# Kernel tuning notes

Hardware: AMD Instinct MI355X
Metric: run time of the kernel (lower is better)

Reference implementation:

```python
import jax, jax.numpy as jnp
from jax import lax
import numpy as np

# Model hyperparameters (match init_kwargs)
DIM = 128
D_STATE = 16
D_CONV = 4
EXPAND = 2
NSLICES = 4
D_INNER = DIM * EXPAND        # 256
DT_RANK = DIM // 16           # 8
B_SZ, H_IMG, W_IMG = 2, 64, 64


def setup_inputs() -> dict:
    key = jax.random.key(0)
    ks = jax.random.split(key, 32)
    def nrm(i, shape, s=0.02):
        return jax.random.normal(ks[i], shape, jnp.float32) * s
    A_init = jnp.log(jnp.tile(jnp.arange(1, D_STATE + 1, dtype=jnp.float32)[None, :], (D_INNER, 1)))
    inp = {}
    inp["x"] = jax.random.normal(ks[0], (B_SZ, DIM, H_IMG, W_IMG), jnp.float32)
    inp["ln_w"] = jnp.ones((DIM,), jnp.float32)
    inp["ln_b"] = jnp.zeros((DIM,), jnp.float32)
    inp["in_proj_w"] = nrm(1, (2 * D_INNER, DIM))
    i = 2
    for s in ("f", "b", "s"):
        inp[f"conv_w_{s}"] = nrm(i, (D_INNER, 1, D_CONV), 0.1); i += 1
        inp[f"conv_b_{s}"] = jnp.zeros((D_INNER,), jnp.float32)
        inp[f"xproj_w_{s}"] = nrm(i, (DT_RANK + 2 * D_STATE, D_INNER)); i += 1
        inp[f"dtproj_w_{s}"] = nrm(i, (D_INNER, DT_RANK), 0.1); i += 1
        inp[f"dtproj_b_{s}"] = nrm(i, (D_INNER,), 0.1) - 4.0; i += 1  # softplus -> small dt
        inp[f"A_log_{s}"] = A_init
        inp[f"D_{s}"] = jnp.ones((D_INNER,), jnp.float32)
    inp["out_proj_w"] = nrm(i, (DIM, D_INNER)); i += 1
    inp["fuse1_w"] = nrm(i, (DIM, 2 * DIM, 3, 3), 0.05); i += 1
    inp["fuse1_b"] = jnp.zeros((DIM,), jnp.float32)
    inp["fuse2_w"] = nrm(i, (DIM, 2 * DIM, 3, 3), 0.05); i += 1
    inp["fuse2_b"] = jnp.zeros((DIM,), jnp.float32)
    return inp


def causal_conv1d(u, w, b):
    # u: (B, L, d); depthwise causal conv over L, kernel (d, 1, K)
    xc = jnp.swapaxes(u, 1, 2)  # (B, d, L)
    xc = jnp.pad(xc, ((0, 0), (0, 0), (w.shape[-1] - 1, 0)))
    y = lax.conv_general_dilated(xc, w, (1,), 'VALID',
                                 dimension_numbers=('NCH', 'OIH', 'NCH'),
                                 feature_group_count=w.shape[0])
    return jnp.swapaxes(y, 1, 2) + b


def selective_scan(u, delta, A, Bm, Cm, D):
    # u, delta: (B, L, d); A: (d, n); Bm, Cm: (B, L, n)
    dA = jnp.exp(delta[..., None] * A)                       # (B, L, d, n)
    dBu = (delta * u)[..., None] * Bm[:, :, None, :]         # (B, L, d, n)
    dA = jnp.moveaxis(dA, 1, 0)                              # (L, B, d, n)
    dBu = jnp.moveaxis(dBu, 1, 0)
    def step(h, xs):
        a, bu = xs
        h = a * h + bu
        return h, h
    h0 = jnp.zeros(dA.shape[1:], dA.dtype)
    _, hs = lax.scan(step, h0, (dA, dBu))                    # hs: (L, B, d, n)
    y = jnp.einsum('lbdn,bln->bld', hs, Cm)
    return y + u * D


def mamba_branch(u, cw, cb, xw, dw, db, A_log, D):
    # u: (B, L, d_inner)
    uc = jax.nn.silu(causal_conv1d(u, cw, cb))
    proj = uc @ xw.T                                         # (B, L, dt_rank + 2*n)
    dt = proj[..., :DT_RANK]
    Bm = proj[..., DT_RANK:DT_RANK + D_STATE]
    Cm = proj[..., DT_RANK + D_STATE:]
    delta = jax.nn.softplus(dt @ dw.T + db)
    return selective_scan(uc, delta, -jnp.exp(A_log), Bm, Cm, D)


def conv2d_3x3(x, w, b):
    y = lax.conv_general_dilated(x, w, (1, 1), ((1, 1), (1, 1)),
                                 dimension_numbers=('NCHW', 'OIHW', 'NCHW'))
    return y + b[None, :, None, None]


def reference(x, ln_w, ln_b, in_proj_w,
              conv_w_f, conv_b_f, xproj_w_f, dtproj_w_f, dtproj_b_f, A_log_f, D_f,
              conv_w_b, conv_b_b, xproj_w_b, dtproj_w_b, dtproj_b_b, A_log_b, D_b,
              conv_w_s, conv_b_s, xproj_w_s, dtproj_w_s, dtproj_b_s, A_log_s, D_s,
              out_proj_w, fuse1_w, fuse1_b, fuse2_w, fuse2_b):
    Bn, C, H, W = x.shape
    L = H * W
    xf = jnp.swapaxes(x.reshape(Bn, C, L), 1, 2)             # (B, L, C)
    mu = xf.mean(-1, keepdims=True)
    var = xf.var(-1, keepdims=True)
    xn = (xf - mu) / jnp.sqrt(var + 1e-5) * ln_w + ln_b
    xz = xn @ in_proj_w.T                                    # (B, L, 2*d_inner)
    u, z = xz[..., :D_INNER], xz[..., D_INNER:]
    # bimamba v3: forward, backward, and slice-permuted scans
    perm = jnp.arange(L).reshape(NSLICES, L // NSLICES).T.reshape(-1)
    inv = jnp.argsort(perm)
    y_f = mamba_branch(u, conv_w_f, conv_b_f, xproj_w_f, dtproj_w_f, dtproj_b_f, A_log_f, D_f)
    y_b = mamba_branch(u[:, ::-1], conv_w_b, conv_b_b, xproj_w_b, dtproj_w_b, dtproj_b_b, A_log_b, D_b)[:, ::-1]
    y_s = mamba_branch(u[:, perm], conv_w_s, conv_b_s, xproj_w_s, dtproj_w_s, dtproj_b_s, A_log_s, D_s)[:, inv]
    q, k, v = y_f, y_b, y_s                                  # (B, L, d_inner) each
    y = (y_f + y_b + y_s) * jax.nn.silu(z)
    out = y @ out_proj_w.T                                   # (B, L, dim)
    # channel-wise global attention: (q^T k) softmax over channels, then v @ attn^T
    attn = jax.nn.softmax(jnp.einsum('bld,ble->bde', q, k), axis=-1)  # (B, D, D)
    out_a = jnp.einsum('bld,bed->ble', v, attn)              # (B, L, d_inner)
    out_a = out_a.reshape(Bn, -1, H, W)                      # matches torch .view(B,-1,H,W)
    out_a = conv2d_3x3(out_a, fuse1_w, fuse1_b)              # (B, dim, H, W)
    out_m = jnp.swapaxes(out, 1, 2).reshape(Bn, C, H, W)
    o = conv2d_3x3(jnp.concatenate([out_a, out_m], axis=1), fuse2_w, fuse2_b)
    return o + x
```

## Files before the change

### kernel.cpp

```cpp
#include <hip/hip_runtime.h>
#include <math.h>

#define B_SZ 2
#define CDIM 128
#define LSEQ 4096
#define DIN  256
#define NPROJ 40
#define NCH  128
#define CHL  (LSEQ / NCH)
#define KSPL 32

typedef float f32x4 __attribute__((ext_vector_type(4)));
typedef short s16x8 __attribute__((ext_vector_type(8)));

__device__ __forceinline__ float silu_f(float v) { return v / (1.f + __expf(-v)); }

__device__ __forceinline__ unsigned short f2bf(float x) {
  unsigned int u = __float_as_uint(x);
  u += 0x7fff + ((u >> 16) & 1);
  return (unsigned short)(u >> 16);
}

__global__ __launch_bounds__(256) void ln_kernel(const float* __restrict__ x,
                                                 const float* __restrict__ w,
                                                 const float* __restrict__ b,
                                                 unsigned short* __restrict__ xnbf) {
  int tile = blockIdx.x;
  int bb = tile >> 6, t0 = (tile & 63) * 64;
  int tid = threadIdx.x;
  __shared__ float sx[128][65];
  #pragma unroll
  for (int i = 0; i < 32; ++i) {
    int idx = tid + i * 256;
    int c = idx >> 6, l = idx & 63;
    sx[c][l] = x[((size_t)bb * 128 + c) * 4096 + t0 + l];
  }
  __syncthreads();
  int row = tid >> 2, part = tid & 3;
  float s = 0.f, s2 = 0.f;
  #pragma unroll 8
  for (int j = 0; j < 32; ++j) { float v = sx[part * 32 + j][row]; s += v; s2 += v * v; }
  s += __shfl_xor(s, 1); s += __shfl_xor(s, 2);
  s2 += __shfl_xor(s2, 1); s2 += __shfl_xor(s2, 2);
  float mu = s * (1.f / 128.f);
  float rstd = rsqrtf(s2 * (1.f / 128.f) - mu * mu + 1e-5f);
  unsigned short* o = xnbf + ((size_t)bb * 4096 + t0 + row) * 128 + part * 32;
  #pragma unroll
  for (int j = 0; j < 32; j += 2) {
    int c = part * 32 + j;
    float v0 = (sx[c][row] - mu) * rstd * w[c] + b[c];
    float v1 = (sx[c + 1][row] - mu) * rstd * w[c + 1] + b[c + 1];
    unsigned int pk = (unsigned int)f2bf(v0) | ((unsigned int)f2bf(v1) << 16);
    *(unsigned int*)(o + j) = pk;
  }
}

__global__ void cvt_bf16(const float* __restrict__ src, unsigned short* __restrict__ dst, int n) {
  int i = blockIdx.x * 256 + threadIdx.x;
  if (i < n) dst[i] = f2bf(src[i]);
}

__global__ void wpack_bf16(const float* __restrict__ a, const float* __restrict__ b,
                           const float* __restrict__ c, unsigned short* __restrict__ dst) {
  int i = blockIdx.x * 256 + threadIdx.x;
  if (i >= 3 * 64 * 256) return;
  int dir = i >> 14, rem = i & 16383;
  int row = rem >> 8, ci = rem & 255;
  const float* s = dir == 0 ? a : dir == 1 ? b : c;
  float v = row < NPROJ ? s[row * 256 + ci] : 0.f;
  dst[i] = f2bf(v);
}

__global__ __launch_bounds__(256) void gemm_mfma_nt(
    const unsigned short* __restrict__ A, const unsigned short* __restrict__ Bm,
    float* __restrict__ C, int M, int N, int K,
    long sAb, long sBb, long sCb) {
  A += (long)blockIdx.z * sAb; Bm += (long)blockIdx.z * sBb; C += (long)blockIdx.z * sCb;
  int m0 = blockIdx.x * 64, n0 = blockIdx.y * 64;
  int tid = threadIdx.x;
  int wv = tid >> 6, lane = tid & 63, col = lane & 15, g = lane >> 4;
  __shared__ unsigned short As[8192];
  __shared__ unsigned short Bs[8192];
  f32x4 acc[4] = {};
  for (int k0 = 0; k0 < K; k0 += 128) {
    __syncthreads();
    #pragma unroll
    for (int i = 0; i < 4; ++i) {
      int s = tid + i * 256;
      int m = s >> 4, kg = s & 15;
      int off = (m * 256 + kg * 16) ^ ((m & 7) << 4);
      uint4 va = *(const uint4*)(A + (size_t)(m0 + m) * K + k0 + kg * 8);
      *(uint4*)((char*)As + off) = va;
      uint4 vb = *(const uint4*)(Bm + (size_t)(n0 + m) * K + k0 + kg * 8);
      *(uint4*)((char*)Bs + off) = vb;
    }
    __syncthreads();
    #pragma unroll
    for (int ks = 0; ks < 4; ++ks) {
      int arow = wv * 16 + col;
      s16x8 a = *(const s16x8*)((const char*)As +
                 ((arow * 256 + ks * 64 + g * 16) ^ ((col & 7) << 4)));
      #pragma unroll
      for (int nf = 0; nf < 4; ++nf) {
        int brow = nf * 16 + col;
        s16x8 bf = *(const s16x8*)((const char*)Bs +
                   ((brow * 256 + ks * 64 + g * 16) ^ ((col & 7) << 4)));
        acc[nf] = __builtin_amdgcn_mfma_f32_16x16x32_bf16(a, bf, acc[nf], 0, 0, 0);
      }
    }
  }
  #pragma unroll
  for (int nf = 0; nf < 4; ++nf) {
    #pragma unroll
    for (int r = 0; r < 4; ++r) {
      int m = m0 + wv * 16 + g * 4 + r;
      int n = n0 + nf * 16 + col;
      if (n < N) C[(size_t)m * N + n] = acc[nf][r];
    }
  }
}

__global__ __launch_bounds__(256) void gemm_tn_splitk(
    const float* __restrict__ A, const float* __restrict__ Bm, float* __restrict__ P) {
  int bz = blockIdx.z;
  int b = bz / KSPL, s = bz % KSPL;
  const float* Ab = A + (size_t)b * LSEQ * DIN + (size_t)s * (LSEQ / KSPL) * DIN;
  const float* Bb = Bm + (size_t)b * LSEQ * DIN + (size_t)s * (LSEQ / KSPL) * DIN;
  float* Pb = P + (size_t)bz * 65536;
  __shared__ float As[32][64];
  __shared__ float Bs[32][64];
  int t = threadIdx.x;
  int m0 = blockIdx.x * 64, n0 = blockIdx.y * 64;
  int tx = t & 15, ty = t >> 4;
  float acc[4][4] = {};
  for (int k0 = 0; k0 < LSEQ / KSPL; k0 += 32) {
    __syncthreads();
    #pragma unroll
    for (int i = 0; i < 8; ++i) {
      int idx = t + i * 256;
      int kk = idx >> 6, m = idx & 63;
      As[kk][m] = Ab[(size_t)(k0 + kk) * DIN + m0 + m];
      Bs[kk][m] = Bb[(size_t)(k0 + kk) * DIN + n0 + m];
    }
    __syncthreads();
    #pragma unroll
    for (int kk = 0; kk < 32; ++kk) {
      float a0[4], b0[4];
      #pragma unroll
      for (int i = 0; i < 4; ++i) a0[i] = As[kk][ty * 4 + i];
      #pragma unroll
      for (int j = 0; j < 4; ++j) b0[j] = Bs[kk][tx * 4 + j];
      #pragma unroll
      for (int i = 0; i < 4; ++i)
        #pragma unroll
        for (int j = 0; j < 4; ++j) acc[i][j] += a0[i] * b0[j];
    }
  }
  #pragma unroll
  for (int i = 0; i < 4; ++i)
    #pragma unroll
    for (int j = 0; j < 4; ++j)
      Pb[(size_t)(m0 + ty * 4 + i) * 256 + n0 + tx * 4 + j] = acc[i][j];
}

__global__ __launch_bounds__(256) void attn_reduce_softmax(
    const float* __restrict__ P, unsigned short* __restrict__ attnbf) {
  int row = blockIdx.x;
  int b = row >> 8, d = row & 255;
  int t = threadIdx.x;
  const float* p = P + ((size_t)b * KSPL) * 65536 + (size_t)d * 256 + t;
  float v = 0.f;
  #pragma unroll
  for (int s = 0; s < KSPL; ++s) v += p[(size_t)s * 65536];
  __shared__ float red[256];
  red[t] = v; __syncthreads();
  for (int s = 128; s > 0; s >>= 1) { if (t < s) red[t] = fmaxf(red[t], red[t + s]); __syncthreads(); }
  float mx = red[0]; __syncthreads();
  float e = __expf(v - mx);
  red[t] = e; __syncthreads();
  for (int s = 128; s > 0; s >>= 1) { if (t < s) red[t] += red[t + s]; __syncthreads(); }
  attnbf[(size_t)row * 256 + t] = f2bf(e / red[0]);
}

__global__ __launch_bounds__(256) void conv1d_silu(const float* __restrict__ xz,
    const float* __restrict__ cw0, const float* __restrict__ cw1, const float* __restrict__ cw2,
    const float* __restrict__ cb0, const float* __restrict__ cb1, const float* __restrict__ cb2,
    float* __restrict__ uc, unsigned short* __restrict__ ucbf) {
  int lt = blockIdx.x, b = blockIdx.y, dir = blockIdx.z;
  int d = threadIdx.x;
  int l0 = lt * 16;
  const float* cw = dir == 0 ? cw0 : dir == 1 ? cw1 : cw2;
  const float* cb = dir == 0 ? cb0 : dir == 1 ? cb1 : cb2;
  float c0 = cw[d * 4], c1 = cw[d * 4 + 1], c2 = cw[d * 4 + 2], c3 = cw[d * 4 + 3];
  float bias = cb[d];
  const float* xp = xz + (size_t)b * LSEQ * 512 + d;
  auto ld = [&](int j) -> float {
    if (j < 0) return 0.f;
    int jm = dir == 0 ? j : dir == 1 ? (LSEQ - 1 - j) : ((j & 3) * 1024 + (j >> 2));
    return xp[(size_t)jm * 512];
  };
  float v0 = ld(l0 - 3), v1 = ld(l0 - 2), v2 = ld(l0 - 1), v3;
  size_t ob = (((size_t)dir * B_SZ + b) * LSEQ + l0) * DIN + d;
  #pragma unroll
  for (int i = 0; i < 16; ++i) {
    v3 = ld(l0 + i);
    float acc = bias + c0 * v0 + c1 * v1 + c2 * v2 + c3 * v3;
    float r = silu_f(acc);
    uc[ob + (size_t)i * DIN] = r;
    ucbf[ob + (size_t)i * DIN] = f2bf(r);
    v0 = v1; v1 = v2; v2 = v3;
  }
}

__global__ __launch_bounds__(256) void scan_part1(
    const float* __restrict__ uc, const float* __restrict__ proj,
    const float* __restrict__ al0, const float* __restrict__ al1, const float* __restrict__ al2,
    const float* __restrict__ dw0, const float* __restrict__ dw1, const float* __restrict__ dw2,
    const float* __restrict__ db0, const float* __restrict__ db1, const float* __restrict__ db2,
    float* __restrict__ hend, float* __restrict__ sdsum) {
  int chunk = blockIdx.x, b = blockIdx.y, dir = blockIdx.z;
  int d = threadIdx.x;
  const float* alog = dir == 0 ? al0 : dir == 1 ? al1 : al2;
  const float* dwp  = dir == 0 ? dw0 : dir == 1 ? dw1 : dw2;
  const float* dbp  = dir == 0 ? db0 : dir == 1 ? db1 : db2;
  float An0 = -__expf(alog[d * 16]) * 1.44269504f;
  float dwr[8];
  #pragma unroll
  for (int i = 0; i < 8; ++i) dwr[i] = dwp[d * 8 + i];
  float dbv = dbp[d];
  size_t base = (((size_t)dir * B_SZ + b) * LSEQ + (size_t)chunk * CHL);
  const float* ucp = uc + base * DIN + d;
  const float* prj = proj + base * NPROJ;
  __shared__ float sPr[CHL][NPROJ];
  for (int i = threadIdx.x; i < CHL * NPROJ; i += 256)
    sPr[i / NPROJ][i % NPROJ] = prj[i];
  __syncthreads();
  float h[16];
  #pragma unroll
  for (int n = 0; n < 16; ++n) h[n] = 0.f;
  float sd = 0.f;
  float uv = ucp[0];
  for (int l = 0; l < CHL; ++l) {
    float uvn = (l + 1 < CHL) ? ucp[(size_t)(l + 1) * DIN] : 0.f;
    float a = dbv;
    #pragma unroll
    for (int i = 0; i < 8; ++i) a += sPr[l][i] * dwr[i];
    float dv = a > 20.f ? a : __logf(1.f + __expf(a));
    sd += dv;
    float du = dv * uv;
    float p = exp2f(dv * An0);
    float p2 = p * p, p4 = p2 * p2;
    float dA0 = p, dA1 = p2, dA2 = p2 * p, dA3 = p4;
    const float4* bp = (const float4*)&sPr[l][8];
    #pragma unroll
    for (int q = 0; q < 4; ++q) {
      float4 bb = bp[q];
      h[q*4+0] = dA0 * h[q*4+0] + du * bb.x;
      h[q*4+1] = dA1 * h[q*4+1] + du * bb.y;
      h[q*4+2] = dA2 * h[q*4+2] + du * bb.z;
      h[q*4+3] = dA3 * h[q*4+3] + du * bb.w;
      if (q < 3) { dA0 *= p4; dA1 *= p4; dA2 *= p4; dA3 *= p4; }
    }
    uv = uvn;
  }
  size_t so = (((size_t)(dir * B_SZ + b) * NCH + chunk) * DIN + d);
  float4* hp = (float4*)(hend + so * 16);
  #pragma unroll
  for (int q = 0; q < 4; ++q) hp[q] = make_float4(h[q*4+0], h[q*4+1], h[q*4+2], h[q*4+3]);
  sdsum[so] = sd;
}

__global__ __launch_bounds__(256) void scan_combine(
    const float* __restrict__ sdsum,
    const float* __restrict__ al0, const float* __restrict__ al1, const float* __restrict__ al2,
    float* __restrict__ hend) {
  int b = blockIdx.y, dir = blockIdx.z;
  int t = threadIdx.x, g = t >> 4, n = t & 15;
  int d = blockIdx.x * 16 + g;
  const float* alog = dir == 0 ? al0 : dir == 1 ? al1 : al2;
  float A2 = -__expf(alog[d * 16 + n]) * 1.44269504f;
  float h = 0.f;
  for (int c = 0; c < NCH; ++c) {
    size_t so = (((size_t)(dir * B_SZ + b) * NCH + c) * DIN + d);
    float old = hend[so * 16 + n];
    float prod = exp2f(sdsum[so] * A2);
    hend[so * 16 + n] = h;
    h = prod * h + old;
  }
}

__global__ __launch_bounds__(256) void scan_part3(
    const float* __restrict__ uc, const float* __restrict__ proj,
    const float* __restrict__ hin,
    const float* __restrict__ al0, const float* __restrict__ al1, const float* __restrict__ al2,
    const float* __restrict__ dw0, const float* __restrict__ dw1, const float* __restrict__ dw2,
    const float* __restrict__ db0, const float* __restrict__ db1, const float* __restrict__ db2,
    const float* __restrict__ D0, const float* __restrict__ D1, const float* __restrict__ D2,
    float* __restrict__ y, unsigned short* __restrict__ ysbf) {
  int chunk = blockIdx.x, b = blockIdx.y, dir = blockIdx.z;
  int d = threadIdx.x;
  const float* alog = dir == 0 ? al0 : dir == 1 ? al1 : al2;
  const float* dwp  = dir == 0 ? dw0 : dir == 1 ? dw1 : dw2;
  const float* dbp  = dir == 0 ? db0 : dir == 1 ? db1 : db2;
  const float* Dp   = dir == 0 ? D0 : dir == 1 ? D1 : D2;
  float An0 = -__expf(alog[d * 16]) * 1.44269504f;
  float dwr[8];
  #pragma unroll
  for (int i = 0; i < 8; ++i) dwr[i] = dwp[d * 8 + i];
  float dbv = dbp[d];
  float Dd = Dp[d];
  size_t base0 = ((size_t)dir * B_SZ + b) * LSEQ;
  size_t base = base0 + (size_t)chunk * CHL;
  const float* ucp = uc + base * DIN + d;
  const float* prj = proj + base * NPROJ;
  float* yp = y + base0 * DIN;
  __shared__ float sPr[CHL][NPROJ];
  for (int i = threadIdx.x; i < CHL * NPROJ; i += 256)
    sPr[i / NPROJ][i % NPROJ] = prj[i];
  __syncthreads();
  size_t so = (((size_t)(dir * B_SZ + b) * NCH + chunk) * DIN + d);
  float h[16];
  const float4* hp = (const float4*)(hin + so * 16);
  #pragma unroll
  for (int q = 0; q < 4; ++q) { float4 v = hp[q]; h[q*4+0]=v.x; h[q*4+1]=v.y; h[q*4+2]=v.z; h[q*4+3]=v.w; }
  float uv = ucp[0];
  for (int l = 0; l < CHL; ++l) {
    float uvn = (l + 1 < CHL) ? ucp[(size_t)(l + 1) * DIN] : 0.f;
    float a = dbv;
    #pragma unroll
    for (int i = 0; i < 8; ++i) a += sPr[l][i] * dwr[i];
    float dv = a > 20.f ? a : __logf(1.f + __expf(a));
    float du = dv * uv;
    float p = exp2f(dv * An0);
    float p2 = p * p, p4 = p2 * p2;
    float dA0 = p, dA1 = p2, dA2 = p2 * p, dA3 = p4;
    const float4* bp = (const float4*)&sPr[l][8];
    const float4* cp = (const float4*)&sPr[l][24];
    float acc0 = 0.f, acc1 = 0.f, acc2 = 0.f, acc3 = 0.f;
    #pragma unroll
    for (int q = 0; q < 4; ++q) {
      float4 bb = bp[q]; float4 cc = cp[q];
      float h0 = dA0 * h[q*4+0] + du * bb.x;
      float h1 = dA1 * h[q*4+1] + du * bb.y;
      float h2 = dA2 * h[q*4+2] + du * bb.z;
      float h3 = dA3 * h[q*4+3] + du * bb.w;
      acc0 += h0 * cc.x; acc1 += h1 * cc.y; acc2 += h2 * cc.z; acc3 += h3 * cc.w;
      h[q*4+0] = h0; h[q*4+1] = h1; h[q*4+2] = h2; h[q*4+3] = h3;
      if (q < 3) { dA0 *= p4; dA1 *= p4; dA2 *= p4; dA3 *= p4; }
    }
    float yv = (acc0 + acc1) + (acc2 + acc3) + uv * Dd;
    int gl = chunk * CHL + l;
    int fl = dir == 0 ? gl : dir == 1 ? (LSEQ - 1 - gl) : ((gl & 3) * 1024 + (gl >> 2));
    yp[(size_t)fl * DIN + d] = yv;
    if (dir == 2) ysbf[((size_t)b * LSEQ + fl) * DIN + d] = f2bf(yv);
    uv = uvn;
  }
}

__global__ void combine_kernel(const float* __restrict__ y, const float* __restrict__ xz,
                               unsigned short* __restrict__ ycombbf) {
  size_t i = ((size_t)blockIdx.x * 256 + threadIdx.x) * 4;
  size_t row = i >> 8;
  int dd = (int)(i & 255);
  const size_t ds = (size_t)B_SZ * LSEQ * DIN;
  float4 a = *(const float4*)(y + i);
  float4 bq = *(const float4*)(y + ds + i);
  float4 c = *(const float4*)(y + 2 * ds + i);
  const float4 z = *(const float4*)(xz + row * 512 + 256 + dd);
  float v0 = (a.x + bq.x + c.x) * silu_f(z.x);
  float v1 = (a.y + bq.y + c.y) * silu_f(z.y);
  float v2 = (a.z + bq.z + c.z) * silu_f(z.z);
  float v3 = (a.w + bq.w + c.w) * silu_f(z.w);
  unsigned int p0 = (unsigned int)f2bf(v0) | ((unsigned int)f2bf(v1) << 16);
  unsigned int p1 = (unsigned int)f2bf(v2) | ((unsigned int)f2bf(v3) << 16);
  *(uint2*)(ycombbf + i) = make_uint2(p0, p1);
}

__global__ void pad_bf16(const float* __restrict__ p1, const float* __restrict__ p2,
                         long p1b, long p2b, unsigned short* __restrict__ dst) {
  int idx = blockIdx.x * 256 + threadIdx.x;
  if (idx >= B_SZ * 66 * 66 * 32) return;
  int cg = idx & 31;
  int pos = idx >> 5;
  int ww = pos % 66; int rest = pos / 66;
  int hh = rest % 66; int b = rest / 66;
  unsigned int pk[4] = {0, 0, 0, 0};
  if (hh != 0 && hh != 65 && ww != 0 && ww != 65) {
    int sp = (hh - 1) * 64 + (ww - 1);
    #pragma unroll
    for (int j = 0; j < 8; ++j) {
      int ci = cg * 8 + j;
      const float* p = ci < 128 ? p1 + (size_t)b * p1b + (size_t)ci * 4096
                                : p2 + (size_t)b * p2b + (size_t)(ci - 128) * 4096;
      unsigned int h16 = f2bf(p[sp]);
      pk[j >> 1] |= h16 << ((j & 1) * 16);
    }
  }
  uint4 v = make_uint4(pk[0], pk[1], pk[2], pk[3]);
  *(uint4*)(dst + (size_t)pos * 256 + cg * 8) = v;
}

__global__ void pad_half(const float* __restrict__ om, unsigned short* __restrict__ dst) {
  int idx = blockIdx.x * 256 + threadIdx.x;
  if (idx >= B_SZ * 4096 * 16) return;
  int cg = idx & 15;
  int pos = idx >> 4;
  int sp = pos & 4095, b = pos >> 12;
  int h = sp >> 6, w = sp & 63;
  const float* s = om + ((size_t)b * 4096 + sp) * 128 + cg * 8;
  float4 a = *(const float4*)s;
  float4 c = *(const float4*)(s + 4);
  unsigned int p0 = (unsigned int)f2bf(a.x) | ((unsigned int)f2bf(a.y) << 16);
  unsigned int p1 = (unsigned int)f2bf(a.z) | ((unsigned int)f2bf(a.w) << 16);
  unsigned int p2 = (unsigned int)f2bf(c.x) | ((unsigned int)f2bf(c.y) << 16);
  unsigned int p3 = (unsigned int)f2bf(c.z) | ((unsigned int)f2bf(c.w) << 16);
  size_t o = (((size_t)b * 66 + h + 1) * 66 + (w + 1)) * 256 + 128 + cg * 8;
  *(uint4*)(dst + o) = make_uint4(p0, p1, p2, p3);
}

__global__ void wcvt_kernel(const float* __restrict__ w, unsigned short* __restrict__ wb) {
  int idx = blockIdx.x * 256 + threadIdx.x;
  int co = idx >> 8, ci = idx & 255;
  const float* s = w + (size_t)idx * 9;
  #pragma unroll
  for (int k = 0; k < 9; ++k)
    wb[((size_t)k * 128 + co) * 256 + ci] = f2bf(s[k]);
}

__global__ __launch_bounds__(256) void conv_mfma(
    const unsigned short* __restrict__ inpad, const unsigned short* __restrict__ Wb,
    const float* __restrict__ bias, const float* __restrict__ resid,
    float* __restrict__ outf, unsigned short* __restrict__ outbf, int mode) {
  int h = blockIdx.x;
  int cohalf = blockIdx.y >> 1, whalf = blockIdx.y & 1;
  int b = blockIdx.z;
  int tid = threadIdx.x;
  int wv = tid >> 6, lane = tid & 63;
  int col = lane & 15, g = lane >> 4;
  int co0 = cohalf * 64 + wv * 16;
  int w0 = whalf * 32;
  __shared__ unsigned short lds[3 * 34 * 64];
  f32x4 acc[2] = {};
  for (int cb = 0; cb < 4; ++cb) {
    __syncthreads();
    for (int s = tid; s < 816; s += 256) {
      int row = s / 272; int rem = s % 272; int c = rem >> 3; int cig = rem & 7;
      const unsigned short* gp = inpad +
          ((((size_t)b * 66 + h + row) * 66 + (w0 + c)) * 256 + cb * 64 + cig * 8);
      uint4 v = *(const uint4*)gp;
      int byte_off = ((row * 34 + c) * 128 + cig * 16) ^ ((c & 7) << 4);
      *(uint4*)((char*)lds + byte_off) = v;
    }
    __syncthreads();
    #pragma unroll
    for (int tap = 0; tap < 9; ++tap) {
      int kh = tap / 3, kw = tap % 3;
      #pragma unroll
      for (int ci0 = 0; ci0 < 64; ci0 += 32) {
        const unsigned short* ap = Wb +
            (((size_t)tap * 128 + co0 + col) * 256 + cb * 64 + ci0 + g * 8);
        s16x8 a = *(const s16x8*)ap;
        #pragma unroll
        for (int t = 0; t < 2; ++t) {
          int c = kw + t * 16 + col;
          int byte_off = ((kh * 34 + c) * 128 + (ci0 + g * 8) * 2) ^ ((c & 7) << 4);
          s16x8 bf = *(const s16x8*)((const char*)lds + byte_off);
          acc[t] = __builtin_amdgcn_mfma_f32_16x16x32_bf16(a, bf, acc[t], 0, 0, 0);
        }
      }
    }
  }
  if (mode == 0) {
    #pragma unroll
    for (int t = 0; t < 2; ++t) {
      #pragma unroll
      for (int r = 0; r < 4; ++r) {
        int co = co0 + g * 4 + r;
        int w = w0 + t * 16 + col;
        size_t o = (((size_t)b * 128 + co) * 4096) + h * 64 + w;
        float v = acc[t][r] + bias[co];
        if (resid) v += resid[o];
        outf[o] = v;
      }
    }
  } else {
    #pragma unroll
    for (int t = 0; t < 2; ++t) {
      int w = w0 + t * 16 + col;
      float v0 = acc[t][0] + bias[co0 + g * 4];
      float v1 = acc[t][1] + bias[co0 + g * 4 + 1];
      float v2 = acc[t][2] + bias[co0 + g * 4 + 2];
      float v3 = acc[t][3] + bias[co0 + g * 4 + 3];
      unsigned int q0 = (unsigned int)f2bf(v0) | ((unsigned int)f2bf(v1) << 16);
      unsigned int q1 = (unsigned int)f2bf(v2) | ((unsigned int)f2bf(v3) << 16);
      size_t o = (((size_t)b * 66 + h + 1) * 66 + (w + 1)) * 256 + co0 + g * 4;
      *(uint2*)(outbf + o) = make_uint2(q0, q1);
    }
  }
}

extern "C" void kernel_launch(void* const* d_in, const int* in_sizes, int n_in,
                              void* d_out, int out_size, void* d_ws, size_t ws_size,
                              hipStream_t stream) {
  const float* x        = (const float*)d_in[0];
  const float* ln_w     = (const float*)d_in[1];
  const float* ln_b     = (const float*)d_in[2];
  const float* in_proj  = (const float*)d_in[3];
  const float* cw[3]  = {(const float*)d_in[4],  (const float*)d_in[11], (const float*)d_in[18]};
  const float* cb[3]  = {(const float*)d_in[5],  (const float*)d_in[12], (const float*)d_in[19]};
  const float* xw[3]  = {(const float*)d_in[6],  (const float*)d_in[13], (const float*)d_in[20]};
  const float* dw[3]  = {(const float*)d_in[7],  (const float*)d_in[14], (const float*)d_in[21]};
  const float* db[3]  = {(const float*)d_in[8],  (const float*)d_in[15], (const float*)d_in[22]};
  const float* al[3]  = {(const float*)d_in[9],  (const float*)d_in[16], (const float*)d_in[23]};
  const float* Dp[3]  = {(const float*)d_in[10], (const float*)d_in[17], (const float*)d_in[24]};
  const float* out_proj = (const float*)d_in[25];
  const float* f1w = (const float*)d_in[26];
  const float* f1b = (const float*)d_in[27];
  const float* f2w = (const float*)d_in[28];
  const float* f2b = (const float*)d_in[29];
  float* out = (float*)d_out;

  float* ws = (float*)d_ws;
  unsigned short* xnbf = (unsigned short*)ws;
  unsigned short* wipb = (unsigned short*)(ws + 524288);
  unsigned short* wopb = (unsigned short*)(ws + 557056);
  unsigned short* Wb1  = (unsigned short*)(ws + 573440);
  unsigned short* Wb2  = (unsigned short*)(ws + 720896);
  unsigned short* xwpackbf = (unsigned short*)(ws + 868352);
  float* xz    = ws + 1048576;
  float* uc    = ws + 5242880;
  float* attP  = uc;
  unsigned short* ycombbf = (unsigned short*)(uc + 4194304);
  unsigned short* inpad1 = (unsigned short*)uc;
  unsigned short* inpad2 = (unsigned short*)(uc + 1115136);
  float* proj  = ws + 11534336;
  float* hend  = ws + 12517376;
  float* out_m  = hend;
  float* out_a  = hend + 1048576;
  unsigned short* attnbf = (unsigned short*)(hend + 3145728);
  float* y     = ws + 18808832;
  unsigned short* ucbf = (unsigned short*)y;
  float* sdsum = ws + 25100288;
  unsigned short* ysbf   = (unsigned short*)(ws + 25296896);

  const long dirUC = (long)B_SZ * LSEQ * DIN;
  const long dirPJ = (long)B_SZ * LSEQ * NPROJ;

  ln_kernel<<<dim3(B_SZ * 64), 256, 0, stream>>>(x, ln_w, ln_b, xnbf);
  cvt_bf16<<<dim3(256), 256, 0, stream>>>(in_proj, wipb, 512 * 128);
  cvt_bf16<<<dim3(128), 256, 0, stream>>>(out_proj, wopb, 128 * 256);
  wcvt_kernel<<<dim3(128), 256, 0, stream>>>(f1w, Wb1);
  wcvt_kernel<<<dim3(128), 256, 0, stream>>>(f2w, Wb2);
  wpack_bf16<<<dim3(192), 256, 0, stream>>>(xw[0], xw[1], xw[2], xwpackbf);
  gemm_mfma_nt<<<dim3(128, 8, 1), 256, 0, stream>>>(xnbf, wipb, xz, 8192, 512, 128, 0, 0, 0);
  conv1d_silu<<<dim3(LSEQ / 16, B_SZ, 3), 256, 0, stream>>>(
      xz, cw[0], cw[1], cw[2], cb[0], cb[1], cb[2], uc, ucbf);
  gemm_mfma_nt<<<dim3(128, 1, 3), 256, 0, stream>>>(ucbf, xwpackbf, proj, 8192, NPROJ, 256,
                                                    dirUC, 64 * 256, dirPJ);
  scan_part1<<<dim3(NCH, B_SZ, 3), 256, 0, stream>>>(uc, proj,
      al[0], al[1], al[2], dw[0], dw[1], dw[2], db[0], db[1], db[2], hend, sdsum);
  scan_combine<<<dim3(16, B_SZ, 3), 256, 0, stream>>>(sdsum, al[0], al[1], al[2], hend);
  scan_part3<<<dim3(NCH, B_SZ, 3), 256, 0, stream>>>(uc, proj, hend,
      al[0], al[1], al[2], dw[0], dw[1], dw[2], db[0], db[1], db[2],
      Dp[0], Dp[1], Dp[2], y, ysbf);
  combine_kernel<<<dim3(B_SZ * LSEQ * DIN / 1024), 256, 0, stream>>>(y, xz, ycombbf);
  gemm_mfma_nt<<<dim3(128, 2, 1), 256, 0, stream>>>(ycombbf, wopb, out_m, 8192, 128, 256, 0, 0, 0);
  gemm_tn_splitk<<<dim3(4, 4, B_SZ * KSPL), 256, 0, stream>>>(y, y + dirUC, attP);
  attn_reduce_softmax<<<dim3(B_SZ * 256), 256, 0, stream>>>(attP, attnbf);
  gemm_mfma_nt<<<dim3(64, 4, B_SZ), 256, 0, stream>>>(ysbf, attnbf, out_a, 4096, 256, 256,
      (long)LSEQ * DIN, 65536, (long)LSEQ * DIN);
  pad_bf16<<<dim3((B_SZ * 66 * 66 * 32 + 255) / 256), 256, 0, stream>>>(
      out_a, out_a + 128 * 4096, (long)LSEQ * DIN, (long)LSEQ * DIN, inpad1);
  hipMemsetAsync(inpad2, 0, (size_t)B_SZ * 66 * 66 * 256 * 2, stream);
  conv_mfma<<<dim3(64, 4, B_SZ), 256, 0, stream>>>(inpad1, Wb1, f1b, nullptr, nullptr, inpad2, 1);
  pad_half<<<dim3((B_SZ * 4096 * 16 + 255) / 256), 256, 0, stream>>>(out_m, inpad2);
  conv_mfma<<<dim3(64, 4, B_SZ), 256, 0, stream>>>(inpad2, Wb2, f2b, x, out, nullptr, 0);
}
```

Measured before the change: 328.2 us.

## Store intermediates in bf16 and merge weight-prep kernels into one launch

The xz projection, conv output, and scan outputs are now stored only as bf16 instead of fp32 or dual fp32+bf16 copies, and every consumer is rewritten to read bf16 (conv1d, scans, combine, split-K attention GEMM). Five weight-conversion launches are fused into one prep kernel, and the split-K factor for the channel-attention GEMM drops from 32 to 16. The workspace layout is rearranged to match. This cuts memory traffic and launch count, at the cost of extra rounding in the scan inputs and the attention logits.

```diff
diff --git a/kernel.cpp b/kernel.cpp
--- a/kernel.cpp
+++ b/kernel.cpp
@@ -8,7 +8,7 @@
 #define NPROJ 40
 #define NCH  128
 #define CHL  (LSEQ / NCH)
-#define KSPL 32
+#define KSPL 16
 
 typedef float f32x4 __attribute__((ext_vector_type(4)));
 typedef short s16x8 __attribute__((ext_vector_type(8)));
@@ -19,6 +19,9 @@
   unsigned int u = __float_as_uint(x);
   u += 0x7fff + ((u >> 16) & 1);
   return (unsigned short)(u >> 16);
+}
+__device__ __forceinline__ float bf2f(unsigned short u) {
+  return __uint_as_float(((unsigned int)u) << 16);
 }
 
 __global__ __launch_bounds__(256) void ln_kernel(const float* __restrict__ x,
@@ -55,27 +58,50 @@
   }
 }
 
-__global__ void cvt_bf16(const float* __restrict__ src, unsigned short* __restrict__ dst, int n) {
-  int i = blockIdx.x * 256 + threadIdx.x;
-  if (i < n) dst[i] = f2bf(src[i]);
-}
-
-__global__ void wpack_bf16(const float* __restrict__ a, const float* __restrict__ b,
-                           const float* __restrict__ c, unsigned short* __restrict__ dst) {
-  int i = blockIdx.x * 256 + threadIdx.x;
-  if (i >= 3 * 64 * 256) return;
-  int dir = i >> 14, rem = i & 16383;
-  int row = rem >> 8, ci = rem & 255;
-  const float* s = dir == 0 ? a : dir == 1 ? b : c;
-  float v = row < NPROJ ? s[row * 256 + ci] : 0.f;
-  dst[i] = f2bf(v);
+__global__ void prep_kernel(const float* __restrict__ in_proj, const float* __restrict__ out_proj,
+                            const float* __restrict__ f1w, const float* __restrict__ f2w,
+                            const float* __restrict__ xw0, const float* __restrict__ xw1,
+                            const float* __restrict__ xw2,
+                            unsigned short* __restrict__ wipb, unsigned short* __restrict__ wopb,
+                            unsigned short* __restrict__ Wb1, unsigned short* __restrict__ Wb2,
+                            unsigned short* __restrict__ xwpackbf) {
+  int bx = blockIdx.x, tid = threadIdx.x;
+  if (bx < 256) {
+    int i = bx * 256 + tid;
+    wipb[i] = f2bf(in_proj[i]);
+  } else if (bx < 384) {
+    int i = (bx - 256) * 256 + tid;
+    wopb[i] = f2bf(out_proj[i]);
+  } else if (bx < 512) {
+    int idx = (bx - 384) * 256 + tid;
+    int co = idx >> 8, ci = idx & 255;
+    const float* s = f1w + (size_t)idx * 9;
+    #pragma unroll
+    for (int k = 0; k < 9; ++k)
+      Wb1[((size_t)k * 128 + co) * 256 + ci] = f2bf(s[k]);
+  } else if (bx < 640) {
+    int idx = (bx - 512) * 256 + tid;
+    int co = idx >> 8, ci = idx & 255;
+    const float* s = f2w + (size_t)idx * 9;
+    #pragma unroll
+    for (int k = 0; k < 9; ++k)
+      Wb2[((size_t)k * 128 + co) * 256 + ci] = f2bf(s[k]);
+  } else {
+    int i = (bx - 640) * 256 + tid;
+    int dir = i >> 14, rem = i & 16383;
+    int row = rem >> 8, ci = rem & 255;
+    const float* s = dir == 0 ? xw0 : dir == 1 ? xw1 : xw2;
+    float v = row < NPROJ ? s[row * 256 + ci] : 0.f;
+    xwpackbf[i] = f2bf(v);
+  }
 }
 
 __global__ __launch_bounds__(256) void gemm_mfma_nt(
     const unsigned short* __restrict__ A, const unsigned short* __restrict__ Bm,
-    float* __restrict__ C, int M, int N, int K,
-    long sAb, long sBb, long sCb) {
-  A += (long)blockIdx.z * sAb; Bm += (long)blockIdx.z * sBb; C += (long)blockIdx.z * sCb;
+    float* __restrict__ C, unsigned short* __restrict__ Cbf, int M, int N, int K,
+    long sAb, long sBb, long sCb, int obf) {
+  A += (long)blockIdx.z * sAb; Bm += (long)blockIdx.z * sBb;
+  if (obf) Cbf += (long)blockIdx.z * sCb; else C += (long)blockIdx.z * sCb;
   int m0 = blockIdx.x * 64, n0 = blockIdx.y * 64;
   int tid = threadIdx.x;
   int wv = tid >> 6, lane = tid & 63, col = lane & 15, g = lane >> 4;
@@ -115,17 +141,20 @@
     for (int r = 0; r < 4; ++r) {
       int m = m0 + wv * 16 + g * 4 + r;
       int n = n0 + nf * 16 + col;
-      if (n < N) C[(size_t)m * N + n] = acc[nf][r];
+      if (n >= N) continue;
+      if (obf) Cbf[(size_t)m * N + n] = f2bf(acc[nf][r]);
+      else     C[(size_t)m * N + n] = acc[nf][r];
     }
   }
 }
 
 __global__ __launch_bounds__(256) void gemm_tn_splitk(
-    const float* __restrict__ A, const float* __restrict__ Bm, float* __restrict__ P) {
+    const unsigned short* __restrict__ A, const unsigned short* __restrict__ Bm,
+    float* __restrict__ P) {
   int bz = blockIdx.z;
   int b = bz / KSPL, s = bz % KSPL;
-  const float* Ab = A + (size_t)b * LSEQ * DIN + (size_t)s * (LSEQ / KSPL) * DIN;
-  const float* Bb = Bm + (size_t)b * LSEQ * DIN + (size_t)s * (LSEQ / KSPL) * DIN;
+  const unsigned short* Ab = A + (size_t)b * LSEQ * DIN + (size_t)s * (LSEQ / KSPL) * DIN;
+  const unsigned short* Bb = Bm + (size_t)b * LSEQ * DIN + (size_t)s * (LSEQ / KSPL) * DIN;
   float* Pb = P + (size_t)bz * 65536;
   __shared__ float As[32][64];
   __shared__ float Bs[32][64];
@@ -135,12 +164,18 @@
   float acc[4][4] = {};
   for (int k0 = 0; k0 < LSEQ / KSPL; k0 += 32) {
     __syncthreads();
-    #pragma unroll
-    for (int i = 0; i < 8; ++i) {
-      int idx = t + i * 256;
+    {
+      int idx = t * 8;
       int kk = idx >> 6, m = idx & 63;
-      As[kk][m] = Ab[(size_t)(k0 + kk) * DIN + m0 + m];
-      Bs[kk][m] = Bb[(size_t)(k0 + kk) * DIN + n0 + m];
+      uint4 va = *(const uint4*)(Ab + (size_t)(k0 + kk) * DIN + m0 + m);
+      uint4 vb = *(const uint4*)(Bb + (size_t)(k0 + kk) * DIN + n0 + m);
+      const unsigned short* pa = (const unsigned short*)&va;
+      const unsigned short* pb = (const unsigned short*)&vb;
+      #pragma unroll
+      for (int j = 0; j < 8; ++j) {
+        As[kk][m + j] = bf2f(pa[j]);
+        Bs[kk][m + j] = bf2f(pb[j]);
+      }
     }
     __syncthreads();
     #pragma unroll
@@ -182,10 +217,10 @@
   attnbf[(size_t)row * 256 + t] = f2bf(e / red[0]);
 }
 
-__global__ __launch_bounds__(256) void conv1d_silu(const float* __restrict__ xz,
+__global__ __launch_bounds__(256) void conv1d_silu(const unsigned short* __restrict__ xz,
     const float* __restrict__ cw0, const float* __restrict__ cw1, const float* __restrict__ cw2,
     const float* __restrict__ cb0, const float* __restrict__ cb1, const float* __restrict__ cb2,
-    float* __restrict__ uc, unsigned short* __restrict__ ucbf) {
+    unsigned short* __restrict__ ucbf) {
   int lt = blockIdx.x, b = blockIdx.y, dir = blockIdx.z;
   int d = threadIdx.x;
   int l0 = lt * 16;
@@ -193,11 +228,11 @@
   const float* cb = dir == 0 ? cb0 : dir == 1 ? cb1 : cb2;
   float c0 = cw[d * 4], c1 = cw[d * 4 + 1], c2 = cw[d * 4 + 2], c3 = cw[d * 4 + 3];
   float bias = cb[d];
-  const float* xp = xz + (size_t)b * LSEQ * 512 + d;
+  const unsigned short* xp = xz + (size_t)b * LSEQ * 512 + d;
   auto ld = [&](int j) -> float {
     if (j < 0) return 0.f;
     int jm = dir == 0 ? j : dir == 1 ? (LSEQ - 1 - j) : ((j & 3) * 1024 + (j >> 2));
-    return xp[(size_t)jm * 512];
+    return bf2f(xp[(size_t)jm * 512]);
   };
   float v0 = ld(l0 - 3), v1 = ld(l0 - 2), v2 = ld(l0 - 1), v3;
   size_t ob = (((size_t)dir * B_SZ + b) * LSEQ + l0) * DIN + d;
@@ -205,15 +240,13 @@
   for (int i = 0; i < 16; ++i) {
     v3 = ld(l0 + i);
     float acc = bias + c0 * v0 + c1 * v1 + c2 * v2 + c3 * v3;
-    float r = silu_f(acc);
-    uc[ob + (size_t)i * DIN] = r;
-    ucbf[ob + (size_t)i * DIN] = f2bf(r);
+    ucbf[ob + (size_t)i * DIN] = f2bf(silu_f(acc));
     v0 = v1; v1 = v2; v2 = v3;
   }
 }
 
 __global__ __launch_bounds__(256) void scan_part1(
-    const float* __restrict__ uc, const float* __restrict__ proj,
+    const unsigned short* __restrict__ uc, const float* __restrict__ proj,
     const float* __restrict__ al0, const float* __restrict__ al1, const float* __restrict__ al2,
     const float* __restrict__ dw0, const float* __restrict__ dw1, const float* __restrict__ dw2,
     const float* __restrict__ db0, const float* __restrict__ db1, const float* __restrict__ db2,
@@ -229,7 +262,7 @@
   for (int i = 0; i < 8; ++i) dwr[i] = dwp[d * 8 + i];
   float dbv = dbp[d];
   size_t base = (((size_t)dir * B_SZ + b) * LSEQ + (size_t)chunk * CHL);
-  const float* ucp = uc + base * DIN + d;
+  const unsigned short* ucp = uc + base * DIN + d;
   const float* prj = proj + base * NPROJ;
   __shared__ float sPr[CHL][NPROJ];
   for (int i = threadIdx.x; i < CHL * NPROJ; i += 256)
@@ -239,9 +272,9 @@
   #pragma unroll
   for (int n = 0; n < 16; ++n) h[n] = 0.f;
   float sd = 0.f;
-  float uv = ucp[0];
+  float uv = bf2f(ucp[0]);
   for (int l = 0; l < CHL; ++l) {
-    float uvn = (l + 1 < CHL) ? ucp[(size_t)(l + 1) * DIN] : 0.f;
+    float uvn = (l + 1 < CHL) ? bf2f(ucp[(size_t)(l + 1) * DIN]) : 0.f;
     float a = dbv;
     #pragma unroll
     for (int i = 0; i < 8; ++i) a += sPr[l][i] * dwr[i];
@@ -290,13 +323,13 @@
 }
 
 __global__ __launch_bounds__(256) void scan_part3(
-    const float* __restrict__ uc, const float* __restrict__ proj,
+    const unsigned short* __restrict__ uc, const float* __restrict__ proj,
     const float* __restrict__ hin,
     const float* __restrict__ al0, const float* __restrict__ al1, const float* __restrict__ al2,
     const float* __restrict__ dw0, const float* __restrict__ dw1, const float* __restrict__ dw2,
     const float* __restrict__ db0, const float* __restrict__ db1, const float* __restrict__ db2,
     const float* __restrict__ D0, const float* __restrict__ D1, const float* __restrict__ D2,
-    float* __restrict__ y, unsigned short* __restrict__ ysbf) {
+    unsigned short* __restrict__ ybf) {
   int chunk = blockIdx.x, b = blockIdx.y, dir = blockIdx.z;
   int d = threadIdx.x;
   const float* alog = dir == 0 ? al0 : dir == 1 ? al1 : al2;
@@ -311,9 +344,9 @@
   float Dd = Dp[d];
   size_t base0 = ((size_t)dir * B_SZ + b) * LSEQ;
   size_t base = base0 + (size_t)chunk * CHL;
-  const float* ucp = uc + base * DIN + d;
+  const unsigned short* ucp = uc + base * DIN + d;
   const float* prj = proj + base * NPROJ;
-  float* yp = y + base0 * DIN;
+  unsigned short* yp = ybf + base0 * DIN;
   __shared__ float sPr[CHL][NPROJ];
   for (int i = threadIdx.x; i < CHL * NPROJ; i += 256)
     sPr[i / NPROJ][i % NPROJ] = prj[i];
@@ -323,9 +356,9 @@
   const float4* hp = (const float4*)(hin + so * 16);
   #pragma unroll
   for (int q = 0; q < 4; ++q) { float4 v = hp[q]; h[q*4+0]=v.x; h[q*4+1]=v.y; h[q*4+2]=v.z; h[q*4+3]=v.w; }
-  float uv = ucp[0];
+  float uv = bf2f(ucp[0]);
   for (int l = 0; l < CHL; ++l) {
-    float uvn = (l + 1 < CHL) ? ucp[(size_t)(l + 1) * DIN] : 0.f;
+    float uvn = (l + 1 < CHL) ? bf2f(ucp[(size_t)(l + 1) * DIN]) : 0.f;
     float a = dbv;
     #pragma unroll
     for (int i = 0; i < 8; ++i) a += sPr[l][i] * dwr[i];
@@ -351,29 +384,34 @@
     float yv = (acc0 + acc1) + (acc2 + acc3) + uv * Dd;
     int gl = chunk * CHL + l;
     int fl = dir == 0 ? gl : dir == 1 ? (LSEQ - 1 - gl) : ((gl & 3) * 1024 + (gl >> 2));
-    yp[(size_t)fl * DIN + d] = yv;
-    if (dir == 2) ysbf[((size_t)b * LSEQ + fl) * DIN + d] = f2bf(yv);
+    yp[(size_t)fl * DIN + d] = f2bf(yv);
     uv = uvn;
   }
 }
 
-__global__ void combine_kernel(const float* __restrict__ y, const float* __restrict__ xz,
+__global__ void combine_kernel(const unsigned short* __restrict__ ybf,
+                               const unsigned short* __restrict__ xz,
                                unsigned short* __restrict__ ycombbf) {
-  size_t i = ((size_t)blockIdx.x * 256 + threadIdx.x) * 4;
+  size_t i = ((size_t)blockIdx.x * 256 + threadIdx.x) * 8;
   size_t row = i >> 8;
   int dd = (int)(i & 255);
   const size_t ds = (size_t)B_SZ * LSEQ * DIN;
-  float4 a = *(const float4*)(y + i);
-  float4 bq = *(const float4*)(y + ds + i);
-  float4 c = *(const float4*)(y + 2 * ds + i);
-  const float4 z = *(const float4*)(xz + row * 512 + 256 + dd);
-  float v0 = (a.x + bq.x + c.x) * silu_f(z.x);
-  float v1 = (a.y + bq.y + c.y) * silu_f(z.y);
-  float v2 = (a.z + bq.z + c.z) * silu_f(z.z);
-  float v3 = (a.w + bq.w + c.w) * silu_f(z.w);
-  unsigned int p0 = (unsigned int)f2bf(v0) | ((unsigned int)f2bf(v1) << 16);
-  unsigned int p1 = (unsigned int)f2bf(v2) | ((unsigned int)f2bf(v3) << 16);
-  *(uint2*)(ycombbf + i) = make_uint2(p0, p1);
+  uint4 va = *(const uint4*)(ybf + i);
+  uint4 vb = *(const uint4*)(ybf + ds + i);
+  uint4 vc = *(const uint4*)(ybf + 2 * ds + i);
+  uint4 vz = *(const uint4*)(xz + row * 512 + 256 + dd);
+  const unsigned short* pa = (const unsigned short*)&va;
+  const unsigned short* pb = (const unsigned short*)&vb;
+  const unsigned short* pc = (const unsigned short*)&vc;
+  const unsigned short* pz = (const unsigned short*)&vz;
+  unsigned int o[4];
+  #pragma unroll
+  for (int j = 0; j < 8; j += 2) {
+    float w0 = (bf2f(pa[j]) + bf2f(pb[j]) + bf2f(pc[j])) * silu_f(bf2f(pz[j]));
+    float w1 = (bf2f(pa[j+1]) + bf2f(pb[j+1]) + bf2f(pc[j+1])) * silu_f(bf2f(pz[j+1]));
+    o[j >> 1] = (unsigned int)f2bf(w0) | ((unsigned int)f2bf(w1) << 16);
+  }
+  *(uint4*)(ycombbf + i) = make_uint4(o[0], o[1], o[2], o[3]);
 }
 
 __global__ void pad_bf16(const float* __restrict__ p1, const float* __restrict__ p2,
@@ -416,15 +454,6 @@
   unsigned int p3 = (unsigned int)f2bf(c.z) | ((unsigned int)f2bf(c.w) << 16);
   size_t o = (((size_t)b * 66 + h + 1) * 66 + (w + 1)) * 256 + 128 + cg * 8;
   *(uint4*)(dst + o) = make_uint4(p0, p1, p2, p3);
-}
-
-__global__ void wcvt_kernel(const float* __restrict__ w, unsigned short* __restrict__ wb) {
-  int idx = blockIdx.x * 256 + threadIdx.x;
-  int co = idx >> 8, ci = idx & 255;
-  const float* s = w + (size_t)idx * 9;
-  #pragma unroll
-  for (int k = 0; k < 9; ++k)
-    wb[((size_t)k * 128 + co) * 256 + ci] = f2bf(s[k]);
 }
 
 __global__ __launch_bounds__(256) void conv_mfma(
@@ -527,48 +556,45 @@
   unsigned short* Wb1  = (unsigned short*)(ws + 573440);
   unsigned short* Wb2  = (unsigned short*)(ws + 720896);
   unsigned short* xwpackbf = (unsigned short*)(ws + 868352);
-  float* xz    = ws + 1048576;
-  float* uc    = ws + 5242880;
-  float* attP  = uc;
-  unsigned short* ycombbf = (unsigned short*)(uc + 4194304);
-  unsigned short* inpad1 = (unsigned short*)uc;
-  unsigned short* inpad2 = (unsigned short*)(uc + 1115136);
-  float* proj  = ws + 11534336;
-  float* hend  = ws + 12517376;
-  float* out_m  = hend;
-  float* out_a  = hend + 1048576;
-  unsigned short* attnbf = (unsigned short*)(hend + 3145728);
-  float* y     = ws + 18808832;
-  unsigned short* ucbf = (unsigned short*)y;
-  float* sdsum = ws + 25100288;
-  unsigned short* ysbf   = (unsigned short*)(ws + 25296896);
+  unsigned short* xzbf = (unsigned short*)(ws + 1048576);
+  unsigned short* ucbf = (unsigned short*)(ws + 3145728);
+  float* proj  = ws + 6291456;
+  float* hend  = ws + 7274496;
+  float* sdsum = ws + 10420224;
+  unsigned short* ybf = (unsigned short*)(ws + 10616832);
+  float* attP  = ws + 13762560;
+  unsigned short* ycombbf = (unsigned short*)(ws + 15859712);
+  float* out_m = ws + 16908288;
+  float* out_a = ws + 17956864;
+  unsigned short* attnbf = (unsigned short*)(ws + 20054016);
+  unsigned short* inpad1 = (unsigned short*)(ws + 20119552);
+  unsigned short* inpad2 = (unsigned short*)(ws + 21234688);
 
   const long dirUC = (long)B_SZ * LSEQ * DIN;
   const long dirPJ = (long)B_SZ * LSEQ * NPROJ;
 
   ln_kernel<<<dim3(B_SZ * 64), 256, 0, stream>>>(x, ln_w, ln_b, xnbf);
-  cvt_bf16<<<dim3(256), 256, 0, stream>>>(in_proj, wipb, 512 * 128);
-  cvt_bf16<<<dim3(128), 256, 0, stream>>>(out_proj, wopb, 128 * 256);
-  wcvt_kernel<<<dim3(128), 256, 0, stream>>>(f1w, Wb1);
-  wcvt_kernel<<<dim3(128), 256, 0, stream>>>(f2w, Wb2);
-  wpack_bf16<<<dim3(192), 256, 0, stream>>>(xw[0], xw[1], xw[2], xwpackbf);
-  gemm_mfma_nt<<<dim3(128, 8, 1), 256, 0, stream>>>(xnbf, wipb, xz, 8192, 512, 128, 0, 0, 0);
+  prep_kernel<<<dim3(832), 256, 0, stream>>>(in_proj, out_proj, f1w, f2w,
+      xw[0], xw[1], xw[2], wipb, wopb, Wb1, Wb2, xwpackbf);
+  gemm_mfma_nt<<<dim3(128, 8, 1), 256, 0, stream>>>(xnbf, wipb, nullptr, xzbf,
+      8192, 512, 128, 0, 0, 0, 1);
   conv1d_silu<<<dim3(LSEQ / 16, B_SZ, 3), 256, 0, stream>>>(
-      xz, cw[0], cw[1], cw[2], cb[0], cb[1], cb[2], uc, ucbf);
-  gemm_mfma_nt<<<dim3(128, 1, 3), 256, 0, stream>>>(ucbf, xwpackbf, proj, 8192, NPROJ, 256,
-                                                    dirUC, 64 * 256, dirPJ);
-  scan_part1<<<dim3(NCH, B_SZ, 3), 256, 0, stream>>>(uc, proj,
+      xzbf, cw[0], cw[1], cw[2], cb[0], cb[1], cb[2], ucbf);
+  gemm_mfma_nt<<<dim3(128, 1, 3), 256, 0, stream>>>(ucbf, xwpackbf, proj, nullptr,
+      8192, NPROJ, 256, dirUC, 64 * 256, dirPJ, 0);
+  scan_part1<<<dim3(NCH, B_SZ, 3), 256, 0, stream>>>(ucbf, proj,
       al[0], al[1], al[2], dw[0], dw[1], dw[2], db[0], db[1], db[2], hend, sdsum);
   scan_combine<<<dim3(16, B_SZ, 3), 256, 0, stream>>>(sdsum, al[0], al[1], al[2], hend);
-  scan_part3<<<dim3(NCH, B_SZ, 3), 256, 0, stream>>>(uc, proj, hend,
+  scan_part3<<<dim3(NCH, B_SZ, 3), 256, 0, stream>>>(ucbf, proj, hend,
       al[0], al[1], al[2], dw[0], dw[1], dw[2], db[0], db[1], db[2],
-      Dp[0], Dp[1], Dp[2], y, ysbf);
-  combine_kernel<<<dim3(B_SZ * LSEQ * DIN / 1024), 256, 0, stream>>>(y, xz, ycombbf);
-  gemm_mfma_nt<<<dim3(128, 2, 1), 256, 0, stream>>>(ycombbf, wopb, out_m, 8192, 128, 256, 0, 0, 0);
-  gemm_tn_splitk<<<dim3(4, 4, B_SZ * KSPL), 256, 0, stream>>>(y, y + dirUC, attP);
+      Dp[0], Dp[1], Dp[2], ybf);
+  combine_kernel<<<dim3(B_SZ * LSEQ * DIN / 2048), 256, 0, stream>>>(ybf, xzbf, ycombbf);
+  gemm_mfma_nt<<<dim3(128, 2, 1), 256, 0, stream>>>(ycombbf, wopb, out_m, nullptr,
+      8192, 128, 256, 0, 0, 0, 0);
+  gemm_tn_splitk<<<dim3(4, 4, B_SZ * KSPL), 256, 0, stream>>>(ybf, ybf + dirUC, attP);
   attn_reduce_softmax<<<dim3(B_SZ * 256), 256, 0, stream>>>(attP, attnbf);
-  gemm_mfma_nt<<<dim3(64, 4, B_SZ), 256, 0, stream>>>(ysbf, attnbf, out_a, 4096, 256, 256,
-      (long)LSEQ * DIN, 65536, (long)LSEQ * DIN);
+  gemm_mfma_nt<<<dim3(64, 4, B_SZ), 256, 0, stream>>>(ybf + 2 * dirUC, attnbf, out_a, nullptr,
+      4096, 256, 256, (long)LSEQ * DIN, 65536, (long)LSEQ * DIN, 0);
   pad_bf16<<<dim3((B_SZ * 66 * 66 * 32 + 255) / 256), 256, 0, stream>>>(
       out_a, out_a + 128 * 4096, (long)LSEQ * DIN, (long)LSEQ * DIN, inpad1);
   hipMemsetAsync(inpad2, 0, (size_t)B_SZ * 66 * 66 * 256 * 2, stream);
```

New measurement: 317.4 us. -3.3%, faster.
